# Performance work log

Measured on AMD Instinct MI355X. Metric: run time of the kernel, lower is better.

The kernel has to match this reference:

```python
import jax, jax.numpy as jnp
import numpy as np


def setup_inputs() -> dict:
    key = jax.random.key(0)
    ks = jax.random.split(key, 7)
    E = 768; CH = 3; PS = 16; B = 128; P = 196
    return {
        "x": jax.random.normal(ks[0], (B, P, E), dtype=jnp.float32),
        "We": jax.random.normal(ks[1], (CH * PS * PS, E), dtype=jnp.float32) * (1.0 / np.sqrt(E)),
        "be": jax.random.normal(ks[2], (CH * PS * PS,), dtype=jnp.float32) * 0.01,
        "filter_re": jax.random.normal(ks[3], (1, 1, 1, PS, PS), dtype=jnp.float32),
        "filter_im": jax.random.normal(ks[4], (1, 1, 1, PS, PS), dtype=jnp.float32),
        "Wd": jax.random.normal(ks[5], (E, CH * PS * PS), dtype=jnp.float32) * (1.0 / np.sqrt(CH * PS * PS)),
        "bd": jax.random.normal(ks[6], (E,), dtype=jnp.float32) * 0.01,
        "ch": 3,
        "patch_size": 16,
    }


def reference(x, We, be, filter_re, filter_im, Wd, bd, ch, patch_size):
    # encode: [b,p,E] -> [b,p,ch*ps*ps]
    h = jnp.einsum('bpe,ce->bpc', x, We) + be
    b, p, _ = h.shape
    h = h.reshape(b, p, ch, patch_size, patch_size)
    # batched 2D FFT over the two trailing patch dims
    hf = jnp.fft.fft2(h, axes=(-2, -1))
    filt = (filter_re + 1j * filter_im).astype(hf.dtype)  # [1,1,1,ps,ps]
    r = jnp.fft.ifft2(hf * filt, axes=(-2, -1))
    a = jnp.abs(r).reshape(b, p, ch * patch_size * patch_size)
    # decode: [b,p,ch*ps*ps] -> [b,p,E]
    return jnp.einsum('bpc,ec->bpe', a, Wd) + bd
```

## Files before the change

kernel.cpp:

```cpp
#include <hip/hip_runtime.h>

typedef short short8 __attribute__((ext_vector_type(8)));
typedef unsigned short ushort8 __attribute__((ext_vector_type(8)));
typedef float f32x4 __attribute__((ext_vector_type(4)));

__device__ __forceinline__ unsigned short f32_to_bf16(float f) {
  unsigned u = __float_as_uint(f);
  unsigned r = 0x7fffu + ((u >> 16) & 1u);
  return (unsigned short)((u + r) >> 16);
}
__device__ __forceinline__ float bf16_to_f32(unsigned short h) {
  return __uint_as_float(((unsigned)h) << 16);
}

__global__ void cvt_f32_bf16(const float* __restrict__ s,
                             unsigned short* __restrict__ d, int n8) {
  int i = blockIdx.x * blockDim.x + threadIdx.x;
  if (i >= n8) return;
  const float4* sp = (const float4*)s;
  float4 a = sp[2 * i], b = sp[2 * i + 1];
  ushort8 o;
  o[0] = f32_to_bf16(a.x); o[1] = f32_to_bf16(a.y);
  o[2] = f32_to_bf16(a.z); o[3] = f32_to_bf16(a.w);
  o[4] = f32_to_bf16(b.x); o[5] = f32_to_bf16(b.y);
  o[6] = f32_to_bf16(b.z); o[7] = f32_to_bf16(b.w);
  ((ushort8*)d)[i] = o;
}

__device__ __forceinline__ void gload_lds16(const void* g, void* l) {
  auto* gp = (const __attribute__((address_space(1))) uint32_t*)((uintptr_t)g);
  auto* lp = (__attribute__((address_space(3))) uint32_t*)(uint32_t)(uintptr_t)l;
  __builtin_amdgcn_global_load_lds(gp, lp, 16, 0, 0);
}

constexpr float C16T[16] = {
    1.f,  0.9238795325112867f,  0.7071067811865476f,  0.3826834323650898f,
    0.f, -0.3826834323650898f, -0.7071067811865476f, -0.9238795325112867f,
   -1.f, -0.9238795325112867f, -0.7071067811865476f, -0.3826834323650898f,
    0.f,  0.3826834323650898f,  0.7071067811865476f,  0.9238795325112867f};
constexpr float S16T[16] = {
    0.f,  0.3826834323650898f,  0.7071067811865476f,  0.9238795325112867f,
    1.f,  0.9238795325112867f,  0.7071067811865476f,  0.3826834323650898f,
    0.f, -0.3826834323650898f, -0.7071067811865476f, -0.9238795325112867f,
   -1.f, -0.9238795325112867f, -0.7071067811865476f, -0.3826834323650898f};

__device__ __forceinline__ void dft16(const float* xr, const float* xi,
                                      float* Xr, float* Xi, const float sgn) {
  float Tr[4][4], Ti[4][4];
#pragma unroll
  for (int c0 = 0; c0 < 4; ++c0) {
    float ar = xr[c0],      ai = xi[c0];
    float br = xr[c0 + 4],  bi = xi[c0 + 4];
    float cr = xr[c0 + 8],  ci = xi[c0 + 8];
    float dr = xr[c0 + 12], di = xi[c0 + 12];
    float Er = ar + cr, Ei = ai + ci, Fr = ar - cr, Fi = ai - ci;
    float Gr = br + dr, Gi = bi + di, Hr = br - dr, Hi = bi - di;
    Tr[c0][0] = Er + Gr; Ti[c0][0] = Ei + Gi;
    Tr[c0][2] = Er - Gr; Ti[c0][2] = Ei - Gi;
    float wHr = -sgn * Hi, wHi = sgn * Hr;
    Tr[c0][1] = Fr + wHr; Ti[c0][1] = Fi + wHi;
    Tr[c0][3] = Fr - wHr; Ti[c0][3] = Fi - wHi;
  }
#pragma unroll
  for (int u = 0; u < 16; ++u) {
    const int m = u & 3;
    float sr = Tr[0][m], si = Ti[0][m];
#pragma unroll
    for (int c0 = 1; c0 < 4; ++c0) {
      const int k = (u * c0) & 15;
      const float wr = C16T[k];
      const float wi = sgn * S16T[k];
      sr += wr * Tr[c0][m] - wi * Ti[c0][m];
      si += wr * Ti[c0][m] + wi * Tr[c0][m];
    }
    Xr[u] = sr; Xi[u] = si;
  }
}

__global__ __launch_bounds__(256) void fold_filter(
    const float* __restrict__ We, const float* __restrict__ be,
    const float* __restrict__ fre, const float* __restrict__ fim,
    unsigned short* __restrict__ Bpp, float* __restrict__ be_re,
    float* __restrict__ be_im) {
  __shared__ float2 S[16 * 276];
  const int tid = threadIdx.x;
  const int p = tid >> 4;
  const int q = tid & 15;
  const int item = blockIdx.x * 16 + p;
  const bool isW = item < 2304;
  const bool isB = (item >= 2304) && (item < 2307);
  const int e = isW ? (item / 3) : 0;
  const int ch = isW ? (item % 3) : (isB ? (item - 2304) : 0);
  const int sb = p * 276;

  {
    float xr[16], xi[16], Xr[16], Xi[16];
#pragma unroll
    for (int c = 0; c < 16; ++c) {
      const int crow = ch * 256 + q * 16 + c;
      xr[c] = isW ? We[(size_t)crow * 768 + e] : be[crow];
      xi[c] = 0.f;
    }
    dft16(xr, xi, Xr, Xi, -1.f);
#pragma unroll
    for (int u = 0; u < 16; ++u) S[sb + q * 17 + u] = make_float2(Xr[u], Xi[u]);
  }
  __syncthreads();

  {
    float xr[16], xi[16], Xr[16], Xi[16];
#pragma unroll
    for (int k = 0; k < 16; ++k) {
      float2 t = S[sb + k * 17 + q];
      xr[k] = t.x; xi[k] = t.y;
    }
    dft16(xr, xi, Xr, Xi, -1.f);
#pragma unroll
    for (int v = 0; v < 16; ++v) {
      float fr = fre[v * 16 + q], fi = fim[v * 16 + q];
      float tr = Xr[v] * fr - Xi[v] * fi;
      float ti = Xr[v] * fi + Xi[v] * fr;
      xr[v] = tr; xi[v] = ti;
    }
    dft16(xr, xi, Xr, Xi, 1.f);
#pragma unroll
    for (int r = 0; r < 16; ++r) S[sb + r * 17 + q] = make_float2(Xr[r], Xi[r]);
  }
  __syncthreads();

  {
    float xr[16], xi[16], Xr[16], Xi[16];
#pragma unroll
    for (int u = 0; u < 16; ++u) {
      float2 t = S[sb + q * 17 + u];
      xr[u] = t.x; xi[u] = t.y;
    }
    dft16(xr, xi, Xr, Xi, 1.f);
#pragma unroll
    for (int c = 0; c < 16; ++c) {
      const int crow = ch * 256 + q * 16 + c;
      const float rr = Xr[c] * (1.f / 256.f);
      const float ri = Xi[c] * (1.f / 256.f);
      if (isW) {
        const size_t rre = (size_t)(crow >> 5) * 64 + (crow & 31);
        Bpp[(rre)*768 + e]      = f32_to_bf16(rr);
        Bpp[(rre + 32)*768 + e] = f32_to_bf16(ri);
      } else if (isB) {
        be_re[crow] = rr;
        be_im[crow] = ri;
      }
    }
  }
}

template <int ENC>
__global__ __launch_bounds__(512, 2) void gemm_d3(
    const unsigned short* __restrict__ A, const unsigned short* __restrict__ B,
    const float* __restrict__ bias_re, const float* __restrict__ bias_im,
    void* __restrict__ out, int M, int K, int nbx) {
  __shared__ __align__(16) unsigned short As[3][256 * 64];
  __shared__ __align__(16) unsigned short Bs[3][128 * 64];

  const int tid = threadIdx.x;
  const int lane = tid & 63;
  const int wid = tid >> 6;
  const int wm = wid >> 1;
  const int wn = wid & 1;

  const int nwg = gridDim.x;
  const int q8 = nwg >> 3, r8 = nwg & 7;
  const int xcd = blockIdx.x & 7, ii = blockIdx.x >> 3;
  const int lid = (xcd < r8 ? xcd * (q8 + 1) : r8 * (q8 + 1) + (xcd - r8) * q8) + ii;
  const int m0 = (lid / nbx) * 256;
  const int n0 = (lid % nbx) * 128;

  const int rr = (wid << 3) + (lane >> 3);
  const int sl = (lane & 7) ^ (lane >> 3);

  f32x4 acc[4][4] = {};

  auto STAGE = [&](int sb, int kt) {
    const int k0 = kt * 64 + sl * 8;
#pragma unroll
    for (int l = 0; l < 4; ++l)
      gload_lds16(A + (size_t)(m0 + l * 64 + rr) * K + k0,
                  &As[sb][(l * 64 + (wid << 3)) * 64]);
#pragma unroll
    for (int l = 0; l < 2; ++l)
      gload_lds16(B + (size_t)(n0 + l * 64 + rr) * K + k0,
                  &Bs[sb][(l * 64 + (wid << 3)) * 64]);
  };

  const int rsel = lane & 15;
  const int swz = (lane & 7) << 4;
  auto COMPUTE = [&](int sb) {
    const char* Ab = (const char*)&As[sb][0];
    const char* Bb = (const char*)&Bs[sb][0];
#pragma unroll
    for (int kk = 0; kk < 2; ++kk) {
      const int kb = (kk * 64 + ((lane >> 4) << 4)) ^ swz;
      short8 af[4], bf[4];
#pragma unroll
      for (int m = 0; m < 4; ++m)
        af[m] = *(const short8*)(Ab + (wm * 64 + m * 16 + rsel) * 128 + kb);
#pragma unroll
      for (int n = 0; n < 4; ++n)
        bf[n] = *(const short8*)(Bb + (wn * 64 + n * 16 + rsel) * 128 + kb);
      __builtin_amdgcn_s_setprio(1);
#pragma unroll
      for (int m = 0; m < 4; ++m)
#pragma unroll
        for (int n = 0; n < 4; ++n)
          acc[m][n] = __builtin_amdgcn_mfma_f32_16x16x32_bf16(
              af[m], bf[n], acc[m][n], 0, 0, 0);
      __builtin_amdgcn_s_setprio(0);
    }
  };

  const int nk = K >> 6;
  STAGE(0, 0);
  STAGE(1, 1);
  for (int kt = 0; kt < nk; ++kt) {
    if (kt < nk - 1)
      asm volatile("s_waitcnt vmcnt(6)" ::: "memory");
    else
      asm volatile("s_waitcnt vmcnt(0)" ::: "memory");
    __builtin_amdgcn_s_barrier();
    asm volatile("" ::: "memory");
    if (kt + 2 < nk) STAGE((kt + 2) % 3, kt + 2);
    COMPUTE(kt % 3);
  }

  const int fr = lane & 15, fq = lane >> 4;
  if (ENC) {
    const int cbase = (n0 + wn * 64) >> 1;
    unsigned short* o = (unsigned short*)out;
#pragma unroll
    for (int n = 0; n < 2; ++n) {
      const int gcol = cbase + n * 16 + fr;
      const float br = bias_re[gcol], bi = bias_im[gcol];
#pragma unroll
      for (int m = 0; m < 4; ++m) {
        const int grow = m0 + wm * 64 + m * 16 + fq * 4;
#pragma unroll
        for (int j = 0; j < 4; ++j) {
          const float re = acc[m][n][j] + br;
          const float im = acc[m][n + 2][j] + bi;
          o[(size_t)(grow + j) * 768 + gcol] =
              f32_to_bf16(sqrtf(re * re + im * im));
        }
      }
    }
  } else {
    float* o = (float*)out;
#pragma unroll
    for (int n = 0; n < 4; ++n) {
      const int gcol = n0 + wn * 64 + n * 16 + fr;
      const float bv = bias_re[gcol];
#pragma unroll
      for (int m = 0; m < 4; ++m) {
        const int grow = m0 + wm * 64 + m * 16 + fq * 4;
#pragma unroll
        for (int j = 0; j < 4; ++j)
          o[(size_t)(grow + j) * 768 + gcol] = acc[m][n][j] + bv;
      }
    }
  }
}

extern "C" void kernel_launch(void* const* d_in, const int* in_sizes, int n_in,
                              void* d_out, int out_size, void* d_ws,
                              size_t ws_size, hipStream_t stream) {
  const float* x   = (const float*)d_in[0];
  const float* We  = (const float*)d_in[1];
  const float* be  = (const float*)d_in[2];
  const float* fre = (const float*)d_in[3];
  const float* fim = (const float*)d_in[4];
  const float* Wd  = (const float*)d_in[5];
  const float* bd  = (const float*)d_in[6];

  const int E = 768, C = 768;
  const int nX = in_sizes[0];
  const int M  = nX / E;
  const int nW = E * C;

  char* w = (char*)d_ws;
  unsigned short* xb    = (unsigned short*)w;
  unsigned short* Wdb   = (unsigned short*)(w + (size_t)nX * 2);
  unsigned short* Bpp   = Wdb + nW;
  float*          be_re = (float*)(Bpp + 2 * (size_t)nW);
  float*          be_im = be_re + C;
  unsigned short* hb    = (unsigned short*)(be_im + C);

  cvt_f32_bf16<<<(nX / 8 + 255) / 256, 256, 0, stream>>>(x, xb, nX / 8);
  cvt_f32_bf16<<<(nW / 8 + 255) / 256, 256, 0, stream>>>(Wd, Wdb, nW / 8);

  fold_filter<<<145, 256, 0, stream>>>(We, be, fre, fim, Bpp, be_re, be_im);

  const int nbx1 = (2 * C) / 128;
  gemm_d3<1><<<nbx1 * (M / 256), 512, 0, stream>>>(xb, Bpp, be_re, be_im, hb,
                                                   M, E, nbx1);

  const int nbx2 = E / 128;
  gemm_d3<0><<<nbx2 * (M / 256), 512, 0, stream>>>(hb, Wdb, bd, nullptr,
                                                   (float*)d_out, M, C, nbx2);
}
```

Baseline: 157.7 us.

## Rework bf16 GEMM into 128x256 tile with interleaved double-buffered schedule

Replaces the triple-buffered 256x128 GEMM with a 128x256 tile and a 2x4 wave layout, using double-buffered LDS. The K loop is split into four barrier-separated phases, each pairing a small set of LDS fragment loads with eight MFMAs, with global-to-LDS stages for the next tiles issued between phases. The aim is finer overlap of memory traffic with MFMA work and a better grid shape for both encode and decode GEMMs. The cost is many more barriers and waitcnts per K step, and pipeline depth drops from three buffers to two.

```diff
diff --git a/kernel.cpp b/kernel.cpp
--- a/kernel.cpp
+++ b/kernel.cpp
@@ -154,82 +154,124 @@
 }
 
 template <int ENC>
-__global__ __launch_bounds__(512, 2) void gemm_d3(
+__global__ __launch_bounds__(512, 2) void gemm_8p(
     const unsigned short* __restrict__ A, const unsigned short* __restrict__ B,
     const float* __restrict__ bias_re, const float* __restrict__ bias_im,
     void* __restrict__ out, int M, int K, int nbx) {
-  __shared__ __align__(16) unsigned short As[3][256 * 64];
-  __shared__ __align__(16) unsigned short Bs[3][128 * 64];
+  __shared__ __align__(16) unsigned short As[2][128 * 64];
+  __shared__ __align__(16) unsigned short Bs[2][256 * 64];
 
   const int tid = threadIdx.x;
   const int lane = tid & 63;
   const int wid = tid >> 6;
-  const int wm = wid >> 1;
-  const int wn = wid & 1;
+  const int wm = wid >> 2;
+  const int wn = wid & 3;
 
   const int nwg = gridDim.x;
   const int q8 = nwg >> 3, r8 = nwg & 7;
   const int xcd = blockIdx.x & 7, ii = blockIdx.x >> 3;
   const int lid = (xcd < r8 ? xcd * (q8 + 1) : r8 * (q8 + 1) + (xcd - r8) * q8) + ii;
-  const int m0 = (lid / nbx) * 256;
-  const int n0 = (lid % nbx) * 128;
-
-  const int rr = (wid << 3) + (lane >> 3);
+  const int m0 = (lid / nbx) * 128;
+  const int n0 = (lid % nbx) * 256;
+
+  const int rA = (wid << 3) + (lane >> 3);
   const int sl = (lane & 7) ^ (lane >> 3);
 
-  f32x4 acc[4][4] = {};
-
-  auto STAGE = [&](int sb, int kt) {
-    const int k0 = kt * 64 + sl * 8;
-#pragma unroll
-    for (int l = 0; l < 4; ++l)
-      gload_lds16(A + (size_t)(m0 + l * 64 + rr) * K + k0,
-                  &As[sb][(l * 64 + (wid << 3)) * 64]);
-#pragma unroll
-    for (int l = 0; l < 2; ++l)
-      gload_lds16(B + (size_t)(n0 + l * 64 + rr) * K + k0,
-                  &Bs[sb][(l * 64 + (wid << 3)) * 64]);
+  char* AsC = (char*)&As[0][0];
+  char* BsC = (char*)&Bs[0][0];
+
+  auto STAGE_A = [&](int buf, int kt) {
+    const unsigned short* g = A + (size_t)(m0 + rA) * K + (kt * 64 + sl * 8);
+    gload_lds16(g, AsC + buf * 16384 + (wid << 10));
+    gload_lds16(g + (size_t)64 * K, AsC + buf * 16384 + 8192 + (wid << 10));
+  };
+  auto STAGE_B = [&](int buf, int kt, int h) {
+    const unsigned short* g =
+        B + (size_t)(n0 + h * 128 + rA) * K + (kt * 64 + sl * 8);
+    gload_lds16(g, BsC + buf * 32768 + h * 16384 + (wid << 10));
+    gload_lds16(g + (size_t)64 * K,
+                BsC + buf * 32768 + h * 16384 + 8192 + (wid << 10));
   };
 
   const int rsel = lane & 15;
   const int swz = (lane & 7) << 4;
-  auto COMPUTE = [&](int sb) {
-    const char* Ab = (const char*)&As[sb][0];
-    const char* Bb = (const char*)&Bs[sb][0];
-#pragma unroll
-    for (int kk = 0; kk < 2; ++kk) {
-      const int kb = (kk * 64 + ((lane >> 4) << 4)) ^ swz;
-      short8 af[4], bf[4];
-#pragma unroll
-      for (int m = 0; m < 4; ++m)
-        af[m] = *(const short8*)(Ab + (wm * 64 + m * 16 + rsel) * 128 + kb);
-#pragma unroll
-      for (int n = 0; n < 4; ++n)
-        bf[n] = *(const short8*)(Bb + (wn * 64 + n * 16 + rsel) * 128 + kb);
-      __builtin_amdgcn_s_setprio(1);
-#pragma unroll
-      for (int m = 0; m < 4; ++m)
-#pragma unroll
-        for (int n = 0; n < 4; ++n)
-          acc[m][n] = __builtin_amdgcn_mfma_f32_16x16x32_bf16(
-              af[m], bf[n], acc[m][n], 0, 0, 0);
-      __builtin_amdgcn_s_setprio(0);
-    }
-  };
+  const int kq = (lane >> 4) << 4;
+
+  short8 af[4], bf0[2], bf1[2];
+  f32x4 acc[4][4] = {};
+
+  auto LD_A = [&](int buf, int kk) {
+    const char* p = AsC + buf * 16384;
+    const int kb = (kk * 64 + kq) ^ swz;
+#pragma unroll
+    for (int m = 0; m < 4; ++m)
+      af[m] = *(const short8*)(p + (wm * 64 + m * 16 + rsel) * 128 + kb);
+  };
+  auto LD_B = [&](int buf, int kk, int np, short8* bf) {
+    const char* p = BsC + buf * 32768;
+    const int kb = (kk * 64 + kq) ^ swz;
+#pragma unroll
+    for (int j = 0; j < 2; ++j)
+      bf[j] = *(const short8*)(p + (wn * 64 + (np * 2 + j) * 16 + rsel) * 128 + kb);
+  };
+  auto MFMA8 = [&](short8* bf, int np) {
+    __builtin_amdgcn_s_setprio(1);
+#pragma unroll
+    for (int m = 0; m < 4; ++m)
+#pragma unroll
+      for (int j = 0; j < 2; ++j)
+        acc[m][np * 2 + j] = __builtin_amdgcn_mfma_f32_16x16x32_bf16(
+            af[m], bf[j], acc[m][np * 2 + j], 0, 0, 0);
+    __builtin_amdgcn_s_setprio(0);
+  };
+
+#define BAR() asm volatile("s_barrier" ::: "memory")
+#define LGKM0()                                         \
+  do {                                                  \
+    asm volatile("s_waitcnt lgkmcnt(0)" ::: "memory");  \
+    __builtin_amdgcn_sched_barrier(0);                  \
+  } while (0)
 
   const int nk = K >> 6;
-  STAGE(0, 0);
-  STAGE(1, 1);
+
+  STAGE_A(0, 0);
+  STAGE_B(0, 0, 0);
+  STAGE_B(0, 0, 1);
+  STAGE_A(1, 1);
+  asm volatile("s_waitcnt vmcnt(2)" ::: "memory");
+  BAR();
+
   for (int kt = 0; kt < nk; ++kt) {
-    if (kt < nk - 1)
-      asm volatile("s_waitcnt vmcnt(6)" ::: "memory");
+    const int buf = kt & 1;
+    const bool s1 = (kt + 1 < nk), s2 = (kt + 2 < nk);
+    LD_A(buf, 0);
+    LD_B(buf, 0, 0, bf0);
+    if (s1) STAGE_B(buf ^ 1, kt + 1, 0);
+    BAR(); LGKM0();
+    MFMA8(bf0, 0);
+    BAR();
+    LD_B(buf, 0, 1, bf1);
+    if (s1) STAGE_B(buf ^ 1, kt + 1, 1);
+    BAR(); LGKM0();
+    MFMA8(bf1, 1);
+    BAR();
+    LD_A(buf, 1);
+    LD_B(buf, 1, 0, bf0);
+    BAR(); LGKM0();
+    MFMA8(bf0, 0);
+    BAR();
+    LD_B(buf, 1, 1, bf1);
+    if (s2) STAGE_A(buf, kt + 2);
+    BAR(); LGKM0();
+    MFMA8(bf1, 1);
+    if (s2)
+      asm volatile("s_waitcnt vmcnt(2)" ::: "memory");
     else
       asm volatile("s_waitcnt vmcnt(0)" ::: "memory");
-    __builtin_amdgcn_s_barrier();
-    asm volatile("" ::: "memory");
-    if (kt + 2 < nk) STAGE((kt + 2) % 3, kt + 2);
-    COMPUTE(kt % 3);
-  }
+    BAR();
+  }
+#undef BAR
+#undef LGKM0
 
   const int fr = lane & 15, fq = lane >> 4;
   if (ENC) {
@@ -297,11 +339,11 @@
 
   fold_filter<<<145, 256, 0, stream>>>(We, be, fre, fim, Bpp, be_re, be_im);
 
-  const int nbx1 = (2 * C) / 128;
-  gemm_d3<1><<<nbx1 * (M / 256), 512, 0, stream>>>(xb, Bpp, be_re, be_im, hb,
+  const int nbx1 = (2 * C) / 256;
+  gemm_8p<1><<<nbx1 * (M / 128), 512, 0, stream>>>(xb, Bpp, be_re, be_im, hb,
                                                    M, E, nbx1);
 
-  const int nbx2 = E / 128;
-  gemm_d3<0><<<nbx2 * (M / 256), 512, 0, stream>>>(hb, Wdb, bd, nullptr,
+  const int nbx2 = E / 256;
+  gemm_8p<0><<<nbx2 * (M / 128), 512, 0, stream>>>(hb, Wdb, bd, nullptr,
                                                    (float*)d_out, M, C, nbx2);
 }
```

Result: slower. 166.6 us (+5.7%).
